# Optimization experiments

Measured on AMD Instinct MI355X. Metric: run time of the kernel, lower is better.

The kernel has to match this reference:

```python
import jax, jax.numpy as jnp
import numpy as np

L, R, H = 4, 4, 16          # left heads, right heads, per-head hidden
D = L * H                    # 64 = left*h = right*h = output_size
B, T = 2, 96


def setup_inputs() -> dict:
    key = jax.random.key(0)
    ks = jax.random.split(key, 16)
    p = lambda k, s: jax.random.normal(k, s, dtype=jnp.float32) * 0.1
    return {
        "queries": jax.random.normal(ks[0], (B, T, D, D), dtype=jnp.float32),
        "keys":    jax.random.normal(ks[1], (B, T, D, D), dtype=jnp.float32),
        "values":  jax.random.normal(ks[2], (B, T, D, D), dtype=jnp.float32),
        "Wq_row": p(ks[3], (D, D)), "Wq_col": p(ks[4], (D, D)), "bq": p(ks[5], (D, D)),
        "Wk_row": p(ks[6], (D, D)), "Wk_col": p(ks[7], (D, D)), "bk": p(ks[8], (D, D)),
        "Wv_row": p(ks[9], (D, D)), "Wv_col": p(ks[10], (D, D)), "bv": p(ks[11], (D, D)),
        "Wo_row": p(ks[12], (D, D)), "Wo_col": p(ks[13], (D, D)), "bo": p(ks[14], (D, D)),
    }


def _pdense(x, Wr, Wc, b):
    # PartialDenseLayer: dense transform on BOTH trailing axes of the 2D token
    # [..., i, j] -> [..., a, b]
    return jnp.einsum('...ij,ia,jb->...ab', x, Wr, Wc) + b


def _separate(x):
    # [B, T, L*H, R*H] -> [B, T, L, R, H, H]
    b, t = x.shape[:2]
    return x.reshape(b, t, L, H, R, H).transpose(0, 1, 2, 4, 3, 5)


def _merge(x):
    # [B, T, L, R, H, H] -> [B, T, L*H, R*H]
    b, t = x.shape[:2]
    return x.transpose(0, 1, 2, 4, 3, 5).reshape(b, t, L * H, R * H)


def reference(queries, keys, values,
              Wq_row, Wq_col, bq, Wk_row, Wk_col, bk,
              Wv_row, Wv_col, bv, Wo_row, Wo_col, bo):
    h = float(H)
    q = _separate(_pdense(queries, Wq_row, Wq_col, bq) / h)  # [B,Tq,L,R,H,H]
    k = _separate(_pdense(keys,    Wk_row, Wk_col, bk) / h)  # [B,Tk,L,R,H,H]
    v = _separate(_pdense(values,  Wv_row, Wv_col, bv) / h)  # [B,Tk,L,R,H,H]
    # similarity_method (method_one): q @ k^T on trailing HxH matrices
    logits = jnp.einsum('bilrpm,bjlrqm->bijlrpq', q, k) / h  # [B,Tq,Tk,L,R,H,H]
    w = jax.nn.softmax(logits, axis=2)                        # softmax over key axis (-5)
    # causal ordering mask over the (L, R) head grid (band_part lower-tri)
    mask = jnp.tril(jnp.ones((L, R), dtype=w.dtype))
    w = w * mask[None, None, None, :, :, None, None]
    # merge_method (method_one): matmul with values then sum over keys
    out = jnp.einsum('bijlrpm,bjlrmq->bilrpq', w, v)          # [B,Tq,L,R,H,H]
    return _pdense(_merge(out), Wo_row, Wo_col, bo) / h       # [B,Tq,D,D]
```

## Files before the change

### kernel.cpp

```cpp
#include <hip/hip_runtime.h>
#include <hip/hip_bf16.h>
#include <math.h>

typedef unsigned int uint32;
typedef __attribute__((ext_vector_type(8))) short s8v;
typedef __attribute__((ext_vector_type(16))) float f16v;
typedef __attribute__((ext_vector_type(2))) unsigned int u2v;

#define LH 4
#define RH 4
#define DD 64
#define BB 2
#define TT 96
#define NTOK (BB*TT)
#define HEADS 16
#define VHEADS 10
#define INV_H 0.0625f
#define LOG2E 1.4426950408889634f
#define ZBLK 96

struct U2 { uint32 x, y; };
struct U4 { uint32 x, y, z, w; };

__device__ __forceinline__ uint32 f2bf(float f) {
    return (uint32)__builtin_bit_cast(unsigned short, __float2bfloat16(f));
}
__device__ __forceinline__ uint32 pkbf(float lo, float hi) {
    return f2bf(lo) | (f2bf(hi) << 16);
}

__device__ __forceinline__ void hswap(uint32 &a, uint32 &b, int h) {
#if __has_builtin(__builtin_amdgcn_permlane32_swap)
    u2v rr = __builtin_amdgcn_permlane32_swap(a, b, false, false);
    a = rr.x; b = rr.y;
#else
    uint32 xa = (uint32)__shfl_xor((int)a, 32, 64);
    uint32 xb = (uint32)__shfl_xor((int)b, 32, 64);
    uint32 na = (h == 0) ? xb : a;
    uint32 nb = (h == 0) ? b  : xa;
    a = na; b = nb;
#endif
}

template<int MODE>
__device__ __forceinline__ void pdense_body(
    const float* __restrict__ Xp,
    const float* __restrict__ Wr, const float* __restrict__ Wc,
    const float* __restrict__ bias, void* __restrict__ dstv,
    float scale, int token, int half)
{
    __shared__ float XsT[64 * 68];
    __shared__ float T1r[64 * 36];

    const int tid = threadIdx.x;
    const int g4 = tid >> 3;
    const int cq = tid & 7;
    const int c0 = half * 32 + cq * 4;

    #pragma unroll
    for (int rep = 0; rep < 32; ++rep) {
        int idx = tid + rep * 128;
        int i = idx >> 6, j = idx & 63;
        XsT[j * 68 + i] = Xp[idx];
    }
    __syncthreads();

    {
        const float4* X4 = (const float4*)XsT;
        float4 a0 = {0,0,0,0}, a1 = {0,0,0,0}, a2 = {0,0,0,0}, a3 = {0,0,0,0};
        #pragma unroll 8
        for (int j = 0; j < 64; ++j) {
            float4 xv = X4[j * 17 + g4];
            float4 wv = *(const float4*)&Wc[j * 64 + c0];
            a0.x = fmaf(xv.x, wv.x, a0.x); a0.y = fmaf(xv.x, wv.y, a0.y);
            a0.z = fmaf(xv.x, wv.z, a0.z); a0.w = fmaf(xv.x, wv.w, a0.w);
            a1.x = fmaf(xv.y, wv.x, a1.x); a1.y = fmaf(xv.y, wv.y, a1.y);
            a1.z = fmaf(xv.y, wv.z, a1.z); a1.w = fmaf(xv.y, wv.w, a1.w);
            a2.x = fmaf(xv.z, wv.x, a2.x); a2.y = fmaf(xv.z, wv.y, a2.y);
            a2.z = fmaf(xv.z, wv.z, a2.z); a2.w = fmaf(xv.z, wv.w, a2.w);
            a3.x = fmaf(xv.w, wv.x, a3.x); a3.y = fmaf(xv.w, wv.y, a3.y);
            a3.z = fmaf(xv.w, wv.z, a3.z); a3.w = fmaf(xv.w, wv.w, a3.w);
        }
        *(float4*)&T1r[(g4 * 4 + 0) * 36 + cq * 4] = a0;
        *(float4*)&T1r[(g4 * 4 + 1) * 36 + cq * 4] = a1;
        *(float4*)&T1r[(g4 * 4 + 2) * 36 + cq * 4] = a2;
        *(float4*)&T1r[(g4 * 4 + 3) * 36 + cq * 4] = a3;
    }
    __syncthreads();

    float4 y0 = {0,0,0,0}, y1 = {0,0,0,0}, y2 = {0,0,0,0}, y3 = {0,0,0,0};
    #pragma unroll 8
    for (int i = 0; i < 64; ++i) {
        float4 wv = *(const float4*)&Wr[i * 64 + g4 * 4];
        float4 tv = *(const float4*)&T1r[i * 36 + cq * 4];
        y0.x = fmaf(wv.x, tv.x, y0.x); y0.y = fmaf(wv.x, tv.y, y0.y);
        y0.z = fmaf(wv.x, tv.z, y0.z); y0.w = fmaf(wv.x, tv.w, y0.w);
        y1.x = fmaf(wv.y, tv.x, y1.x); y1.y = fmaf(wv.y, tv.y, y1.y);
        y1.z = fmaf(wv.y, tv.z, y1.z); y1.w = fmaf(wv.y, tv.w, y1.w);
        y2.x = fmaf(wv.z, tv.x, y2.x); y2.y = fmaf(wv.z, tv.y, y2.y);
        y2.z = fmaf(wv.z, tv.z, y2.z); y2.w = fmaf(wv.z, tv.w, y2.w);
        y3.x = fmaf(wv.w, tv.x, y3.x); y3.y = fmaf(wv.w, tv.y, y3.y);
        y3.z = fmaf(wv.w, tv.z, y3.z); y3.w = fmaf(wv.w, tv.w, y3.w);
    }

    const int bI = token / TT, t = token % TT;
    float z[4][4];
    {
        float4 ys[4] = {y0, y1, y2, y3};
        #pragma unroll
        for (int aa = 0; aa < 4; ++aa) {
            float4 bv = *(const float4*)&bias[(g4 * 4 + aa) * 64 + c0];
            z[aa][0] = (ys[aa].x + bv.x) * scale;
            z[aa][1] = (ys[aa].y + bv.y) * scale;
            z[aa][2] = (ys[aa].z + bv.z) * scale;
            z[aa][3] = (ys[aa].w + bv.w) * scale;
        }
    }

    if (MODE == 0) {
        #pragma unroll
        for (int aa = 0; aa < 4; ++aa) {
            float4 v = {z[aa][0], z[aa][1], z[aa][2], z[aa][3]};
            *(float4*)((float*)dstv + (size_t)token * 4096 + (g4 * 4 + aa) * 64 + c0) = v;
        }
    } else if (MODE == 1) {
        const int r = c0 >> 4, cc = c0 & 15;
        #pragma unroll
        for (int aa = 0; aa < 4; ++aa) {
            int a = g4 * 4 + aa, lh = a >> 4, p = a & 15;
            U2 pk = { pkbf(z[aa][0], z[aa][1]), pkbf(z[aa][2], z[aa][3]) };
            *(U2*)((unsigned short*)dstv +
                   ((size_t)((bI * HEADS + lh * RH + r) * TT + t)) * 256 + p * 16 + cc) = pk;
        }
    } else {
        const int a0i = g4 * 4;
        const int lh = a0i >> 4, m0 = a0i & 15;
        #pragma unroll
        for (int cc2 = 0; cc2 < 4; ++cc2) {
            int cfull = c0 + cc2, r = cfull >> 4, up = cfull & 15;
            U2 pk = { pkbf(z[0][cc2], z[1][cc2]), pkbf(z[2][cc2], z[3][cc2]) };
            *(U2*)((unsigned short*)dstv +
                   ((size_t)((bI * HEADS + lh * RH + r) * TT + t)) * 256 + up * 16 + m0) = pk;
        }
    }
}

__global__ __launch_bounds__(128, 2) void pdense_qkv_kernel(
    const float* __restrict__ Xq, const float* __restrict__ Xk, const float* __restrict__ Xv,
    const float* __restrict__ Wq_row, const float* __restrict__ Wq_col, const float* __restrict__ bq,
    const float* __restrict__ Wk_row, const float* __restrict__ Wk_col, const float* __restrict__ bk,
    const float* __restrict__ Wv_row, const float* __restrict__ Wv_col, const float* __restrict__ bv,
    unsigned short* __restrict__ q_bf, unsigned short* __restrict__ k_bf,
    unsigned short* __restrict__ vt_bf, float* __restrict__ att)
{
    const int bid = blockIdx.x;
    if (bid >= 3 * NTOK * 2) {
        const int zb = bid - 3 * NTOK * 2;
        float4* a4 = (float4*)att;
        #pragma unroll
        for (int k = 0; k < 16; ++k)
            a4[(size_t)zb * 2048 + k * 128 + threadIdx.x] = float4{0.f, 0.f, 0.f, 0.f};
        return;
    }
    const int which = bid / (NTOK * 2);
    const int rem   = bid % (NTOK * 2);
    const int token = rem >> 1, half = rem & 1;

    if (which == 0)
        pdense_body<1>(Xq + (size_t)token * 4096, Wq_row, Wq_col, bq, q_bf,
                       INV_H * INV_H * LOG2E, token, half);
    else if (which == 1)
        pdense_body<1>(Xk + (size_t)token * 4096, Wk_row, Wk_col, bk, k_bf, INV_H, token, half);
    else
        pdense_body<2>(Xv + (size_t)token * 4096, Wv_row, Wv_col, bv, vt_bf, INV_H, token, half);
}

__global__ __launch_bounds__(128, 2) void pdense_out_kernel(
    const float* __restrict__ X, const float* __restrict__ Wr,
    const float* __restrict__ Wc, const float* __restrict__ bias,
    float* __restrict__ dst)
{
    const int token = blockIdx.x >> 1, half = blockIdx.x & 1;
    pdense_body<0>(X + (size_t)token * 4096, Wr, Wc, bias, dst, INV_H, token, half);
}

__global__ __launch_bounds__(256, 4) void attn_kernel(
    const unsigned short* __restrict__ q_bf,
    const unsigned short* __restrict__ k_bf,
    const unsigned short* __restrict__ vt_bf,
    float* __restrict__ att)
{
    __shared__ float lds_z[4][64][9];
    __shared__ float lds_pv[4][64][17];

    const int ip = blockIdx.x % (TT / 2);
    const int vh = (blockIdx.x / (TT / 2)) % VHEADS;
    const int bI = blockIdx.x / ((TT / 2) * VHEADS);
    const int l = (vh >= 1) + (vh >= 3) + (vh >= 6);
    const int r = vh - (l * (l + 1)) / 2;
    const int head = l * RH + r;
    const int i0 = ip * 2;
    const int lane = threadIdx.x & 63;
    const int wv = threadIdx.x >> 6;
    const int c5 = lane & 31;
    const int h  = lane >> 5;

    const size_t hb = (size_t)(bI * HEADS + head) * TT * 256;
    const int frow = (c5 & 15) * 16 + 8 * h;

    s8v qf = *(const s8v*)(q_bf + hb + (size_t)(i0 + (c5 >> 4)) * 256 + frow);
    const unsigned short* kb = k_bf + hb + frow;
    const unsigned short* vb = vt_bf + hb + frow;

    const int jb = wv * (TT / 4);
    const f16v fz16 = {0,0,0,0,0,0,0,0,0,0,0,0,0,0,0,0};

    float ls[8] = {0,0,0,0,0,0,0,0};
    #pragma unroll 3
    for (int jp = 0; jp < 12; ++jp) {
        const int j0g = jb + jp * 2;
        s8v kf = *(const s8v*)(kb + (size_t)(j0g + (c5 >> 4)) * 256);
        f16v d = __builtin_amdgcn_mfma_f32_32x32x16_bf16(kf, qf, fz16, 0, 0, 0);
        #pragma unroll
        for (int t = 0; t < 8; ++t)
            ls[t] += exp2f(d[t]) + exp2f(d[t + 8]);
    }
    #pragma unroll
    for (int t = 0; t < 8; ++t) lds_z[wv][lane][t] = ls[t];
    __syncthreads();
    float inv[8];
    #pragma unroll
    for (int t = 0; t < 8; ++t) {
        float s = lds_z[0][lane][t] + lds_z[1][lane][t]
                + lds_z[2][lane][t] + lds_z[3][lane][t];
        inv[t] = 1.f / s;
    }

    f16v pv = fz16;
    #pragma unroll 2
    for (int jp = 0; jp < 12; ++jp) {
        const int j0g = jb + jp * 2;
        s8v kf = *(const s8v*)(kb + (size_t)(j0g + (c5 >> 4)) * 256);
        f16v d = __builtin_amdgcn_mfma_f32_32x32x16_bf16(kf, qf, fz16, 0, 0, 0);
        float w[16];
        #pragma unroll
        for (int t = 0; t < 8; ++t) {
            w[t]     = exp2f(d[t])     * inv[t];
            w[t + 8] = exp2f(d[t + 8]) * inv[t];
        }
        uint32 A0 = pkbf(w[0],  w[1]),  A1 = pkbf(w[2],  w[3]);
        uint32 A2 = pkbf(w[4],  w[5]),  A3 = pkbf(w[6],  w[7]);
        uint32 B0 = pkbf(w[8],  w[9]),  B1 = pkbf(w[10], w[11]);
        uint32 B2 = pkbf(w[12], w[13]), B3 = pkbf(w[14], w[15]);
        hswap(A2, A0, h); hswap(A3, A1, h);
        hswap(B2, B0, h); hswap(B3, B1, h);
        U4 fa = {A0, A1, A2, A3};
        U4 fb = {B0, B1, B2, B3};
        s8v vf0 = *(const s8v*)(vb + (size_t)(j0g + 0) * 256);
        s8v vf1 = *(const s8v*)(vb + (size_t)(j0g + 1) * 256);
        pv = __builtin_amdgcn_mfma_f32_32x32x16_bf16(__builtin_bit_cast(s8v, fa), vf0, pv, 0, 0, 0);
        pv = __builtin_amdgcn_mfma_f32_32x32x16_bf16(__builtin_bit_cast(s8v, fb), vf1, pv, 0, 0, 0);
    }

    #pragma unroll
    for (int t = 0; t < 16; ++t) lds_pv[wv][lane][t] = pv[t];
    __syncthreads();

    if (c5 < 16) {
        #pragma unroll
        for (int rr = 0; rr < 4; ++rr) {
            const int reg = wv * 4 + rr;
            float v = lds_pv[0][lane][reg] + lds_pv[1][lane][reg]
                    + lds_pv[2][lane][reg] + lds_pv[3][lane][reg];
            const int row = rr + 8 * wv + 4 * h;
            const int i = row >> 4, p = row & 15;
            att[((size_t)(bI * TT + i0 + i) * DD + l * 16 + p) * DD + r * 16 + c5] = v;
        }
    }
}

extern "C" void kernel_launch(void* const* d_in, const int* in_sizes, int n_in,
                              void* d_out, int out_size, void* d_ws, size_t ws_size,
                              hipStream_t stream) {
    const float* queries = (const float*)d_in[0];
    const float* keys    = (const float*)d_in[1];
    const float* values  = (const float*)d_in[2];
    const float* Wq_row  = (const float*)d_in[3];
    const float* Wq_col  = (const float*)d_in[4];
    const float* bq      = (const float*)d_in[5];
    const float* Wk_row  = (const float*)d_in[6];
    const float* Wk_col  = (const float*)d_in[7];
    const float* bk      = (const float*)d_in[8];
    const float* Wv_row  = (const float*)d_in[9];
    const float* Wv_col  = (const float*)d_in[10];
    const float* bv      = (const float*)d_in[11];
    const float* Wo_row  = (const float*)d_in[12];
    const float* Wo_col  = (const float*)d_in[13];
    const float* bo      = (const float*)d_in[14];
    float* out = (float*)d_out;

    const size_t SEP = (size_t)BB * HEADS * TT * 256;
    unsigned short* q_bf  = (unsigned short*)d_ws;
    unsigned short* k_bf  = q_bf + SEP;
    unsigned short* vt_bf = k_bf + SEP;
    float* att = (float*)(vt_bf + SEP);

    pdense_qkv_kernel<<<3 * NTOK * 2 + ZBLK, 128, 0, stream>>>(
        queries, keys, values,
        Wq_row, Wq_col, bq, Wk_row, Wk_col, bk, Wv_row, Wv_col, bv,
        q_bf, k_bf, vt_bf, att);

    attn_kernel<<<BB * VHEADS * (TT / 2), 256, 0, stream>>>(q_bf, k_bf, vt_bf, att);

    pdense_out_kernel<<<NTOK * 2, 128, 0, stream>>>(att, Wo_row, Wo_col, bo, out);
}
```

Before: 66.51 us.

## Move QKV partial-dense projections onto bf16 MFMA with pre-transposed weights

Replaces the fp32 FMA-based Q/K/V partial-dense kernel with one that uses 32x32x16 bf16 MFMA, one wave per token-half, with the column and row transforms as two MFMA stages joined through LDS. A new small kernel runs on every call and converts and transposes the weight matrices to bf16 and transposes the biases so MFMA operands load contiguously. The goal is to cut the FP32 ALU cost of the projections. The cost is an extra kernel launch, an extra bf16 rounding of the intermediate, and scalar 2-byte scattered stores for the outputs.

```diff
diff --git a/kernel.cpp b/kernel.cpp
--- a/kernel.cpp
+++ b/kernel.cpp
@@ -3,6 +3,7 @@
 #include <math.h>
 
 typedef unsigned int uint32;
+typedef unsigned short ushort_t;
 typedef __attribute__((ext_vector_type(8))) short s8v;
 typedef __attribute__((ext_vector_type(16))) float f16v;
 typedef __attribute__((ext_vector_type(2))) unsigned int u2v;
@@ -17,18 +18,21 @@
 #define VHEADS 10
 #define INV_H 0.0625f
 #define LOG2E 1.4426950408889634f
-#define ZBLK 96
+#define QKV_BLOCKS 288
+#define ZF_BLOCKS 48
 
 struct U2 { uint32 x, y; };
 struct U4 { uint32 x, y, z, w; };
 
 __device__ __forceinline__ uint32 f2bf(float f) {
-    return (uint32)__builtin_bit_cast(unsigned short, __float2bfloat16(f));
+    return (uint32)__builtin_bit_cast(ushort_t, __float2bfloat16(f));
 }
 __device__ __forceinline__ uint32 pkbf(float lo, float hi) {
     return f2bf(lo) | (f2bf(hi) << 16);
 }
-
+__device__ __forceinline__ float bf2f(uint32 u) {
+    return __uint_as_float(u << 16);
+}
 __device__ __forceinline__ void hswap(uint32 &a, uint32 &b, int h) {
 #if __has_builtin(__builtin_amdgcn_permlane32_swap)
     u2v rr = __builtin_amdgcn_permlane32_swap(a, b, false, false);
@@ -42,15 +46,143 @@
 #endif
 }
 
-template<int MODE>
-__device__ __forceinline__ void pdense_body(
-    const float* __restrict__ Xp,
-    const float* __restrict__ Wr, const float* __restrict__ Wc,
-    const float* __restrict__ bias, void* __restrict__ dstv,
-    float scale, int token, int half)
+__global__ __launch_bounds__(256) void wprep_kernel(
+    const float* __restrict__ Wq_row, const float* __restrict__ Wq_col, const float* __restrict__ bq,
+    const float* __restrict__ Wk_row, const float* __restrict__ Wk_col, const float* __restrict__ bk,
+    const float* __restrict__ Wv_row, const float* __restrict__ Wv_col, const float* __restrict__ bv,
+    const float* __restrict__ Wo_row, const float* __restrict__ Wo_col, const float* __restrict__ bo,
+    ushort_t* __restrict__ wct, ushort_t* __restrict__ wrt, float* __restrict__ bT)
+{
+    const int task = blockIdx.x;
+    const int tid = threadIdx.x;
+    #pragma unroll
+    for (int e = 0; e < 16; ++e) {
+        const int idx = e * 256 + tid;
+        const int src = (idx & 63) * 64 + (idx >> 6);
+        switch (task) {
+        case 0: wct[idx]          = (ushort_t)f2bf(Wq_col[src]); break;
+        case 1: wct[4096 + idx]   = (ushort_t)f2bf(Wk_col[src]); break;
+        case 2: wct[8192 + idx]   = (ushort_t)f2bf(Wv_col[src]); break;
+        case 3: wrt[idx]          = (ushort_t)f2bf(Wq_row[src]); break;
+        case 4: wrt[4096 + idx]   = (ushort_t)f2bf(Wk_row[src]); break;
+        case 5: wrt[8192 + idx]   = (ushort_t)f2bf(Wv_row[src]); break;
+        case 6: bT[idx]           = bq[src]; break;
+        case 7: bT[4096 + idx]    = bk[src]; break;
+        default: bT[8192 + idx]   = bv[src]; break;
+        }
+    }
+}
+
+__global__ __launch_bounds__(256) void pdense_qkv_mfma(
+    const float* __restrict__ Xq, const float* __restrict__ Xk, const float* __restrict__ Xv,
+    const ushort_t* __restrict__ wct, const ushort_t* __restrict__ wrt,
+    const float* __restrict__ bT,
+    ushort_t* __restrict__ q_bf, ushort_t* __restrict__ k_bf,
+    ushort_t* __restrict__ vt_bf, float* __restrict__ att)
+{
+    __shared__ float lds_t1[4][32][68];
+
+    const int bid = blockIdx.x;
+    if (bid >= QKV_BLOCKS) {
+        const int zb = bid - QKV_BLOCKS;
+        float4* a4 = (float4*)att;
+        #pragma unroll
+        for (int it = 0; it < 16; ++it)
+            a4[(size_t)zb * 4096 + it * 256 + threadIdx.x] = float4{0.f, 0.f, 0.f, 0.f};
+        return;
+    }
+    const int wv = threadIdx.x >> 6;
+    const int task = bid * 4 + wv;
+    const int proj = task / (NTOK * 2);
+    const int rem  = task % (NTOK * 2);
+    const int token = rem >> 1;
+    const int ch = rem & 1;
+    const int lane = threadIdx.x & 63;
+    const int c5 = lane & 31, h = lane >> 5;
+    const int c = ch * 32 + c5;
+    const int bI = token / TT, t = token % TT;
+
+    const float* X = (proj == 0) ? Xq : (proj == 1) ? Xk : Xv;
+    const float* Xp = X + (size_t)token * 4096;
+    const ushort_t* wc = wct + proj * 4096;
+    const ushort_t* wr = wrt + proj * 4096;
+    const float*    bt = bT + proj * 4096;
+    const float scale = (proj == 0) ? (INV_H * INV_H * LOG2E) : INV_H;
+
+    const f16v fz = {0,0,0,0,0,0,0,0,0,0,0,0,0,0,0,0};
+
+    f16v t1_0 = fz, t1_1 = fz;
+    #pragma unroll
+    for (int n = 0; n < 4; ++n) {
+        s8v bf = *(const s8v*)(wc + c * 64 + n * 16 + 8 * h);
+        {
+            const float* xr = Xp + (size_t)c5 * 64 + n * 16 + 8 * h;
+            float4 xa = *(const float4*)xr, xb = *(const float4*)(xr + 4);
+            U4 u = { pkbf(xa.x, xa.y), pkbf(xa.z, xa.w), pkbf(xb.x, xb.y), pkbf(xb.z, xb.w) };
+            t1_0 = __builtin_amdgcn_mfma_f32_32x32x16_bf16(__builtin_bit_cast(s8v, u), bf, t1_0, 0, 0, 0);
+        }
+        {
+            const float* xr = Xp + (size_t)(32 + c5) * 64 + n * 16 + 8 * h;
+            float4 xa = *(const float4*)xr, xb = *(const float4*)(xr + 4);
+            U4 u = { pkbf(xa.x, xa.y), pkbf(xa.z, xa.w), pkbf(xb.x, xb.y), pkbf(xb.z, xb.w) };
+            t1_1 = __builtin_amdgcn_mfma_f32_32x32x16_bf16(__builtin_bit_cast(s8v, u), bf, t1_1, 0, 0, 0);
+        }
+    }
+
+    #pragma unroll
+    for (int tt = 0; tt < 16; ++tt) {
+        const int i = (tt & 3) + 8 * (tt >> 2) + 4 * h;
+        lds_t1[wv][c5][i]      = t1_0[tt];
+        lds_t1[wv][c5][32 + i] = t1_1[tt];
+    }
+    __syncthreads();
+
+    s8v bfr[4];
+    #pragma unroll
+    for (int n = 0; n < 4; ++n) {
+        const float* p = &lds_t1[wv][c5][n * 16 + 8 * h];
+        float4 xa = *(const float4*)p, xb = *(const float4*)(p + 4);
+        U4 u = { pkbf(xa.x, xa.y), pkbf(xa.z, xa.w), pkbf(xb.x, xb.y), pkbf(xb.z, xb.w) };
+        bfr[n] = __builtin_bit_cast(s8v, u);
+    }
+
+    #pragma unroll
+    for (int At = 0; At < 2; ++At) {
+        f16v y = fz;
+        #pragma unroll
+        for (int n = 0; n < 4; ++n) {
+            s8v af = *(const s8v*)(wr + (size_t)(32 * At + c5) * 64 + n * 16 + 8 * h);
+            y = __builtin_amdgcn_mfma_f32_32x32x16_bf16(af, bfr[n], y, 0, 0, 0);
+        }
+        #pragma unroll
+        for (int rg = 0; rg < 4; ++rg) {
+            float4 bv = *(const float4*)(bt + c * 64 + 32 * At + 8 * rg + 4 * h);
+            float be[4] = {bv.x, bv.y, bv.z, bv.w};
+            #pragma unroll
+            for (int e = 0; e < 4; ++e) {
+                const int a = 32 * At + 8 * rg + 4 * h + e;
+                const float val = (y[rg * 4 + e] + be[e]) * scale;
+                const ushort_t ov = (ushort_t)f2bf(val);
+                const size_t base =
+                    ((size_t)((bI * HEADS + (a >> 4) * RH + (c >> 4)) * TT + t)) * 256;
+                if (proj == 0)      q_bf[base + (a & 15) * 16 + (c & 15)] = ov;
+                else if (proj == 1) k_bf[base + (a & 15) * 16 + (c & 15)] = ov;
+                else                vt_bf[base + (c & 15) * 16 + (a & 15)] = ov;
+            }
+        }
+    }
+}
+
+__global__ __launch_bounds__(128, 2) void pdense_out_fp32(
+    const float* __restrict__ Xall, const float* __restrict__ Wr,
+    const float* __restrict__ Wc, const float* __restrict__ bias,
+    float* __restrict__ dst)
 {
     __shared__ float XsT[64 * 68];
     __shared__ float T1r[64 * 36];
+
+    const int token = blockIdx.x >> 1, half = blockIdx.x & 1;
+    const float* Xp = Xall + (size_t)token * 4096;
 
     const int tid = threadIdx.x;
     const int g4 = tid >> 3;
@@ -103,91 +235,22 @@
         y3.z = fmaf(wv.w, tv.z, y3.z); y3.w = fmaf(wv.w, tv.w, y3.w);
     }
 
-    const int bI = token / TT, t = token % TT;
-    float z[4][4];
-    {
-        float4 ys[4] = {y0, y1, y2, y3};
-        #pragma unroll
-        for (int aa = 0; aa < 4; ++aa) {
-            float4 bv = *(const float4*)&bias[(g4 * 4 + aa) * 64 + c0];
-            z[aa][0] = (ys[aa].x + bv.x) * scale;
-            z[aa][1] = (ys[aa].y + bv.y) * scale;
-            z[aa][2] = (ys[aa].z + bv.z) * scale;
-            z[aa][3] = (ys[aa].w + bv.w) * scale;
-        }
-    }
-
-    if (MODE == 0) {
-        #pragma unroll
-        for (int aa = 0; aa < 4; ++aa) {
-            float4 v = {z[aa][0], z[aa][1], z[aa][2], z[aa][3]};
-            *(float4*)((float*)dstv + (size_t)token * 4096 + (g4 * 4 + aa) * 64 + c0) = v;
-        }
-    } else if (MODE == 1) {
-        const int r = c0 >> 4, cc = c0 & 15;
-        #pragma unroll
-        for (int aa = 0; aa < 4; ++aa) {
-            int a = g4 * 4 + aa, lh = a >> 4, p = a & 15;
-            U2 pk = { pkbf(z[aa][0], z[aa][1]), pkbf(z[aa][2], z[aa][3]) };
-            *(U2*)((unsigned short*)dstv +
-                   ((size_t)((bI * HEADS + lh * RH + r) * TT + t)) * 256 + p * 16 + cc) = pk;
-        }
-    } else {
-        const int a0i = g4 * 4;
-        const int lh = a0i >> 4, m0 = a0i & 15;
-        #pragma unroll
-        for (int cc2 = 0; cc2 < 4; ++cc2) {
-            int cfull = c0 + cc2, r = cfull >> 4, up = cfull & 15;
-            U2 pk = { pkbf(z[0][cc2], z[1][cc2]), pkbf(z[2][cc2], z[3][cc2]) };
-            *(U2*)((unsigned short*)dstv +
-                   ((size_t)((bI * HEADS + lh * RH + r) * TT + t)) * 256 + up * 16 + m0) = pk;
-        }
-    }
-}
-
-__global__ __launch_bounds__(128, 2) void pdense_qkv_kernel(
-    const float* __restrict__ Xq, const float* __restrict__ Xk, const float* __restrict__ Xv,
-    const float* __restrict__ Wq_row, const float* __restrict__ Wq_col, const float* __restrict__ bq,
-    const float* __restrict__ Wk_row, const float* __restrict__ Wk_col, const float* __restrict__ bk,
-    const float* __restrict__ Wv_row, const float* __restrict__ Wv_col, const float* __restrict__ bv,
-    unsigned short* __restrict__ q_bf, unsigned short* __restrict__ k_bf,
-    unsigned short* __restrict__ vt_bf, float* __restrict__ att)
-{
-    const int bid = blockIdx.x;
-    if (bid >= 3 * NTOK * 2) {
-        const int zb = bid - 3 * NTOK * 2;
-        float4* a4 = (float4*)att;
-        #pragma unroll
-        for (int k = 0; k < 16; ++k)
-            a4[(size_t)zb * 2048 + k * 128 + threadIdx.x] = float4{0.f, 0.f, 0.f, 0.f};
-        return;
-    }
-    const int which = bid / (NTOK * 2);
-    const int rem   = bid % (NTOK * 2);
-    const int token = rem >> 1, half = rem & 1;
-
-    if (which == 0)
-        pdense_body<1>(Xq + (size_t)token * 4096, Wq_row, Wq_col, bq, q_bf,
-                       INV_H * INV_H * LOG2E, token, half);
-    else if (which == 1)
-        pdense_body<1>(Xk + (size_t)token * 4096, Wk_row, Wk_col, bk, k_bf, INV_H, token, half);
-    else
-        pdense_body<2>(Xv + (size_t)token * 4096, Wv_row, Wv_col, bv, vt_bf, INV_H, token, half);
-}
-
-__global__ __launch_bounds__(128, 2) void pdense_out_kernel(
-    const float* __restrict__ X, const float* __restrict__ Wr,
-    const float* __restrict__ Wc, const float* __restrict__ bias,
-    float* __restrict__ dst)
-{
-    const int token = blockIdx.x >> 1, half = blockIdx.x & 1;
-    pdense_body<0>(X + (size_t)token * 4096, Wr, Wc, bias, dst, INV_H, token, half);
+    float4 ys[4] = {y0, y1, y2, y3};
+    #pragma unroll
+    for (int aa = 0; aa < 4; ++aa) {
+        int a = g4 * 4 + aa;
+        float4 bv = *(const float4*)&bias[a * 64 + c0];
+        float4 v;
+        v.x = (ys[aa].x + bv.x) * INV_H; v.y = (ys[aa].y + bv.y) * INV_H;
+        v.z = (ys[aa].z + bv.z) * INV_H; v.w = (ys[aa].w + bv.w) * INV_H;
+        *(float4*)(dst + (size_t)token * 4096 + a * 64 + c0) = v;
+    }
 }
 
 __global__ __launch_bounds__(256, 4) void attn_kernel(
-    const unsigned short* __restrict__ q_bf,
-    const unsigned short* __restrict__ k_bf,
-    const unsigned short* __restrict__ vt_bf,
+    const ushort_t* __restrict__ q_bf,
+    const ushort_t* __restrict__ k_bf,
+    const ushort_t* __restrict__ vt_bf,
     float* __restrict__ att)
 {
     __shared__ float lds_z[4][64][9];
@@ -209,8 +272,8 @@
     const int frow = (c5 & 15) * 16 + 8 * h;
 
     s8v qf = *(const s8v*)(q_bf + hb + (size_t)(i0 + (c5 >> 4)) * 256 + frow);
-    const unsigned short* kb = k_bf + hb + frow;
-    const unsigned short* vb = vt_bf + hb + frow;
+    const ushort_t* kb = k_bf + hb + frow;
+    const ushort_t* vb = vt_bf + hb + frow;
 
     const int jb = wv * (TT / 4);
     const f16v fz16 = {0,0,0,0,0,0,0,0,0,0,0,0,0,0,0,0};
@@ -300,17 +363,22 @@
     float* out = (float*)d_out;
 
     const size_t SEP = (size_t)BB * HEADS * TT * 256;
-    unsigned short* q_bf  = (unsigned short*)d_ws;
-    unsigned short* k_bf  = q_bf + SEP;
-    unsigned short* vt_bf = k_bf + SEP;
-    float* att = (float*)(vt_bf + SEP);
-
-    pdense_qkv_kernel<<<3 * NTOK * 2 + ZBLK, 128, 0, stream>>>(
-        queries, keys, values,
+    ushort_t* q_bf  = (ushort_t*)d_ws;
+    ushort_t* k_bf  = q_bf + SEP;
+    ushort_t* vt_bf = k_bf + SEP;
+    float*    att   = (float*)(vt_bf + SEP);
+    ushort_t* wct   = (ushort_t*)(att + SEP);
+    ushort_t* wrt   = wct + 3 * 4096;
+    float*    bT    = (float*)(wrt + 3 * 4096);
+
+    wprep_kernel<<<9, 256, 0, stream>>>(
         Wq_row, Wq_col, bq, Wk_row, Wk_col, bk, Wv_row, Wv_col, bv,
-        q_bf, k_bf, vt_bf, att);
+        Wo_row, Wo_col, bo, wct, wrt, bT);
+
+    pdense_qkv_mfma<<<QKV_BLOCKS + ZF_BLOCKS, 256, 0, stream>>>(
+        queries, keys, values, wct, wrt, bT, q_bf, k_bf, vt_bf, att);
 
     attn_kernel<<<BB * VHEADS * (TT / 2), 256, 0, stream>>>(q_bf, k_bf, vt_bf, att);
 
-    pdense_out_kernel<<<NTOK * 2, 128, 0, stream>>>(att, Wo_row, Wo_col, bo, out);
-}
+    pdense_out_fp32<<<NTOK * 2, 128, 0, stream>>>(att, Wo_row, Wo_col, bo, out);
+}
```

After: 65.09 us. 2.1% less time.
